# Kernel tuning notes

Hardware: AMD Instinct MI355X
Metric: run time of the kernel (lower is better)

## Reference

```python
import jax, jax.numpy as jnp
import numpy as np

B = 8192
N_COLS = 64
D = 1024
EPS = 1e-5


def _layernorm(x, g, b):
    m = jnp.mean(x, axis=-1, keepdims=True)
    v = jnp.mean(jnp.square(x - m), axis=-1, keepdims=True)
    return (x - m) * jax.lax.rsqrt(v + EPS) * g + b


def setup_inputs() -> dict:
    key = jax.random.key(0)
    ks = jax.random.split(key, 8)
    s = 0.02
    return {
        "x1_enc": jax.random.normal(ks[0], (1, N_COLS, D), jnp.float32),
        "x2_enc": jax.random.normal(ks[1], (B, D), jnp.float32),
        "We": jax.random.normal(ks[2], (4, 2 * D, D), jnp.float32) * s,
        "be": jnp.zeros((4, D), jnp.float32),
        "W1": jax.random.normal(ks[3], (2 * D, 4 * D), jnp.float32) * s,
        "b1": jnp.zeros((4 * D,), jnp.float32),
        "g1": jnp.ones((4 * D,), jnp.float32),
        "bt1": jnp.zeros((4 * D,), jnp.float32),
        "W2": jax.random.normal(ks[4], (4 * D, 2 * D), jnp.float32) * s,
        "b2": jnp.zeros((2 * D,), jnp.float32),
        "g2": jnp.ones((2 * D,), jnp.float32),
        "bt2": jnp.zeros((2 * D,), jnp.float32),
        "W3": jax.random.normal(ks[5], (2 * D, 1), jnp.float32) * s,
        "b3": jnp.zeros((1,), jnp.float32),
        "col_pairs": jax.random.randint(ks[6], (B, 2), 0, N_COLS, jnp.int64),
        "vis_type": jax.random.randint(ks[7], (B,), 0, 4, jnp.int64),
    }


def reference(x1_enc, x2_enc, We, be, W1, b1, g1, bt1, W2, b2, g2, bt2, W3, b3,
              col_pairs, vis_type):
    # x1 repeated B times is identical per row -> gather directly from x1_enc[0]
    x11 = x1_enc[0, col_pairs[:, 0]]          # [B, D]
    x12 = x1_enc[0, col_pairs[:, 1]]          # [B, D]
    x1c = jnp.concatenate([x11, x12], axis=1)  # [B, 2D]

    # 1-of-4 expert routing: compute all experts, select by vis_type
    all_y = jax.nn.relu(jnp.einsum('bd,edk->bek', x1c, We) + be)  # [B, 4, D]
    y1 = jnp.take_along_axis(all_y, vis_type[:, None, None], axis=1)[:, 0]  # [B, D]

    y = jnp.concatenate([y1, x2_enc], axis=1)  # [B, 2D]
    h = _layernorm(jax.nn.relu(y @ W1 + b1), g1, bt1)
    h = _layernorm(jax.nn.relu(h @ W2 + b2), g2, bt2)
    return jax.nn.sigmoid(h @ W3 + b3)  # [B, 1]
```

## Files before the change

### kernel.cpp

```cpp
#include <hip/hip_runtime.h>

typedef unsigned short u16;
typedef __bf16 bf16x8 __attribute__((ext_vector_type(8)));
typedef float f32x4v __attribute__((ext_vector_type(4)));
typedef u16 u16x8 __attribute__((ext_vector_type(8)));

__device__ __forceinline__ u16 f2bf(float f) {
  union { float f; unsigned u; } v; v.f = f;
  unsigned r = v.u + 0x7fffu + ((v.u >> 16) & 1u);
  return (u16)(r >> 16);
}
__device__ __forceinline__ float bf2f(u16 h) {
  union { unsigned u; float f; } v; v.u = ((unsigned)h) << 16;
  return v.f;
}

#define G2L16(g, l)                                                            \
  __builtin_amdgcn_global_load_lds((__attribute__((address_space(1))) void*)(g), \
                                   (__attribute__((address_space(3))) void*)(l), 16, 0, 0)

__global__ __launch_bounds__(256) void k_transpose2(const float* __restrict__ W1,
                                                    u16* __restrict__ W1T,
                                                    const float* __restrict__ W2,
                                                    u16* __restrict__ W2gT,
                                                    const float* __restrict__ g1,
                                                    const float* __restrict__ bt1,
                                                    float* __restrict__ w2ps,
                                                    float* __restrict__ w2pc) {
  __shared__ float tile[64][65];
  int bid = blockIdx.x;
  const float* in;
  u16* out;
  int R, C, bx, by, fold;
  if (bid < 2048) {
    in = W1; out = W1T; R = 2048; C = 4096; fold = 0;
    bx = bid & 63; by = bid >> 6;
  } else {
    bid -= 2048;
    in = W2; out = W2gT; R = 4096; C = 2048; fold = 1;
    bx = bid & 31; by = bid >> 5;
  }
  const int c0 = bx * 64, r0 = by * 64;
  const int t = threadIdx.x;
  const int tc = (t & 15) * 4, tr = t >> 4;
#pragma unroll
  for (int i = 0; i < 4; ++i) {
    int r = tr + i * 16;
    f32x4v v = *(const f32x4v*)(in + (size_t)(r0 + r) * C + c0 + tc);
    tile[r][tc] = v[0]; tile[r][tc + 1] = v[1];
    tile[r][tc + 2] = v[2]; tile[r][tc + 3] = v[3];
  }
  __syncthreads();
  const int oc = t >> 2;
  const int rb = (t & 3) * 16;
  float gv[16];
#pragma unroll
  for (int i = 0; i < 16; ++i) gv[i] = fold ? g1[r0 + rb + i] : 1.f;
  u16x8 o0, o1;
#pragma unroll
  for (int i = 0; i < 8; ++i) o0[i] = f2bf(tile[rb + i][oc] * gv[i]);
#pragma unroll
  for (int i = 0; i < 8; ++i) o1[i] = f2bf(tile[rb + 8 + i][oc] * gv[8 + i]);
  *(u16x8*)(out + (size_t)(c0 + oc) * R + r0 + rb) = o0;
  *(u16x8*)(out + (size_t)(c0 + oc) * R + r0 + rb + 8) = o1;
  if (fold) {
    float ps = 0.f, pc = 0.f;
#pragma unroll
    for (int i = 0; i < 16; ++i) {
      float w = tile[rb + i][oc];
      ps += gv[i] * w;
      pc += bt1[r0 + rb + i] * w;
    }
    ps += __shfl_down(ps, 2, 4); ps += __shfl_down(ps, 1, 4);
    pc += __shfl_down(pc, 2, 4); pc += __shfl_down(pc, 1, 4);
    if ((t & 3) == 0) {
      w2ps[(size_t)by * 2048 + c0 + oc] = ps;
      w2pc[(size_t)by * 2048 + c0 + oc] = pc;
    }
  }
}

__global__ __launch_bounds__(256) void k_pq(const float* __restrict__ x1,
                                            const float* __restrict__ We,
                                            float* __restrict__ pq0,
                                            float* __restrict__ pq1) {
  const int n0 = blockIdx.x * 64;
  const int ep = blockIdx.y;
  const int e = ep >> 1, p = ep & 1;
  const int khalf = blockIdx.z & 1;
  const int chalf = blockIdx.z >> 1;
  const int ks = khalf * 512;
  float* pq = khalf ? pq1 : pq0;
  __shared__ float As[32][33];
  __shared__ float Bs[32][68];
  const int t = threadIdx.x;
  const int tx = t & 15, ty = t >> 4;
  float acc[2][4] = {};
  const float* wbase = We + (size_t)e * 2048 * 1024 + (size_t)p * 1024 * 1024;
  for (int k0 = ks; k0 < ks + 512; k0 += 32) {
#pragma unroll
    for (int i = 0; i < 4; ++i) {
      int ix = t + i * 256;
      As[ix >> 5][ix & 31] =
          x1[(size_t)(chalf * 32 + (ix >> 5)) * 1024 + k0 + (ix & 31)];
    }
#pragma unroll
    for (int i = 0; i < 8; ++i) {
      int ix = t + i * 256;
      Bs[ix >> 6][ix & 63] = wbase[(size_t)(k0 + (ix >> 6)) * 1024 + n0 + (ix & 63)];
    }
    __syncthreads();
#pragma unroll
    for (int kk = 0; kk < 32; ++kk) {
      float av[2];
#pragma unroll
      for (int i = 0; i < 2; ++i) av[i] = As[ty * 2 + i][kk];
      f32x4v bv = *(const f32x4v*)&Bs[kk][tx * 4];
#pragma unroll
      for (int i = 0; i < 2; ++i)
#pragma unroll
        for (int j = 0; j < 4; ++j) acc[i][j] += av[i] * bv[j];
    }
    __syncthreads();
  }
#pragma unroll
  for (int i = 0; i < 2; ++i) {
    float* dst = pq + ((size_t)ep * 64 + chalf * 32 + ty * 2 + i) * 1024 + n0 + tx * 4;
#pragma unroll
    for (int j = 0; j < 4; ++j) dst[j] = acc[i][j];
  }
}

__global__ __launch_bounds__(256) void k_build_y(const float* __restrict__ pq0,
                                                 const float* __restrict__ pq1,
                                                 const float* __restrict__ x2,
                                                 const float* __restrict__ be,
                                                 const int* __restrict__ cp,
                                                 const int* __restrict__ vis,
                                                 u16* __restrict__ Y) {
  const int t = threadIdx.x;
  for (int rr = 0; rr < 8; ++rr) {
    const int b = blockIdx.x * 8 + rr;
    const int e = vis[b];
    u16x8 o;
    if (t < 128) {
      const int c0 = cp[2 * b], c1 = cp[2 * b + 1];
      const size_t po = ((size_t)(e * 2) * 64 + c0) * 1024 + t * 8;
      const size_t qo = ((size_t)(e * 2 + 1) * 64 + c1) * 1024 + t * 8;
      const float* B = be + e * 1024 + t * 8;
#pragma unroll
      for (int i = 0; i < 8; ++i) {
        float v = pq0[po + i] + pq1[po + i] + pq0[qo + i] + pq1[qo + i] + B[i];
        o[i] = f2bf(v > 0.f ? v : 0.f);
      }
      *(u16x8*)(Y + (size_t)b * 2048 + t * 8) = o;
    } else {
      const float* X = x2 + (size_t)b * 1024 + (size_t)(t - 128) * 8;
#pragma unroll
      for (int i = 0; i < 8; ++i) o[i] = f2bf(X[i]);
      *(u16x8*)(Y + (size_t)b * 2048 + 1024 + (size_t)(t - 128) * 8) = o;
    }
  }
}

template <int MODE>
__global__ __launch_bounds__(256, 3) void k_gemm(const u16* __restrict__ A,
                                                 const u16* __restrict__ BT,
                                                 const float* __restrict__ bias,
                                                 const float2* __restrict__ stats,
                                                 const float* __restrict__ s1,
                                                 const float* __restrict__ c1b,
                                                 const float* __restrict__ gw3,
                                                 float2* __restrict__ sp_out,
                                                 float4* __restrict__ part,
                                                 u16* __restrict__ C,
                                                 int M, int N, int K) {
  __shared__ u16 As[128 * 64];
  __shared__ u16 Bs[128 * 64];
  const int tid = threadIdx.x;
  const int lane = tid & 63;
  const int wave = tid >> 6;

  const int nx = gridDim.x, ny = gridDim.y;
  const int bid = blockIdx.y * nx + blockIdx.x;
  const int stripe = ny >> 3;
  const int xcd = bid & 7;
  const int loc = bid >> 3;
  const int panel = loc / (stripe * 4);
  const int rem = loc - panel * (stripe * 4);
  const int by = xcd * stripe + (rem >> 2);
  const int bx = panel * 4 + (rem & 3);
  const int tileN = bx * 128;
  const int tileM = by * 128;
  const int wm = wave & 1;
  const int wn = wave >> 1;

  f32x4v acc[4][4];
#pragma unroll
  for (int i = 0; i < 4; ++i)
#pragma unroll
    for (int j = 0; j < 4; ++j) acc[i][j] = (f32x4v){0.f, 0.f, 0.f, 0.f};

  const int srow = tid >> 3;
  const int lchunk = (tid & 7) ^ (srow & 7);
  const u16* aptr = A + (size_t)(tileM + srow) * K + lchunk * 8;
  const u16* bptr = BT + (size_t)(tileN + srow) * K + lchunk * 8;
  u16* asp = As + tid * 8;
  u16* bsp = Bs + tid * 8;

  const int s = lane & 7;
  const int kp0 = ((lane >> 4) ^ s) * 8;
  const int kp1 = kp0 ^ 32;
  const int am = wm * 64 + (lane & 15);
  const int bn = wn * 64 + (lane & 15);

  for (int k0 = 0; k0 < K; k0 += 64) {
    G2L16(aptr, asp);
    G2L16(aptr + (size_t)32 * K, asp + 2048);
    G2L16(aptr + (size_t)64 * K, asp + 4096);
    G2L16(aptr + (size_t)96 * K, asp + 6144);
    G2L16(bptr, bsp);
    G2L16(bptr + (size_t)32 * K, bsp + 2048);
    G2L16(bptr + (size_t)64 * K, bsp + 4096);
    G2L16(bptr + (size_t)96 * K, bsp + 6144);
    aptr += 64;
    bptr += 64;
    __syncthreads();

    bf16x8 af[4], bfr[4];
#pragma unroll
    for (int mi = 0; mi < 4; ++mi)
      af[mi] = *(const bf16x8*)(As + (am + mi * 16) * 64 + kp0);
#pragma unroll
    for (int ni = 0; ni < 4; ++ni)
      bfr[ni] = *(const bf16x8*)(Bs + (bn + ni * 16) * 64 + kp0);
#pragma unroll
    for (int mi = 0; mi < 4; ++mi)
#pragma unroll
      for (int ni = 0; ni < 4; ++ni)
        acc[mi][ni] = __builtin_amdgcn_mfma_f32_16x16x32_bf16(af[mi], bfr[ni], acc[mi][ni], 0, 0, 0);
#pragma unroll
    for (int mi = 0; mi < 4; ++mi)
      af[mi] = *(const bf16x8*)(As + (am + mi * 16) * 64 + kp1);
#pragma unroll
    for (int ni = 0; ni < 4; ++ni)
      bfr[ni] = *(const bf16x8*)(Bs + (bn + ni * 16) * 64 + kp1);
#pragma unroll
    for (int mi = 0; mi < 4; ++mi)
#pragma unroll
      for (int ni = 0; ni < 4; ++ni)
        acc[mi][ni] = __builtin_amdgcn_mfma_f32_16x16x32_bf16(af[mi], bfr[ni], acc[mi][ni], 0, 0, 0);
    __syncthreads();
  }

  const int crow = tileM + wm * 64 + (lane >> 4) * 4;
  const int ccol = tileN + wn * 64 + (lane & 15);
  float cv0[4], cv1[4], cg[4];
#pragma unroll
  for (int ni = 0; ni < 4; ++ni) {
    const int c = ccol + ni * 16;
    if (MODE == 0) {
      cv0[ni] = bias[c];
    } else {
      cv0[ni] = s1[c];
      cv1[ni] = c1b[c];
      cg[ni] = gw3[c];
    }
  }
  const int cb = bx * 2 + wn;
#pragma unroll
  for (int mi = 0; mi < 4; ++mi) {
#pragma unroll
    for (int r = 0; r < 4; ++r) {
      const int row = crow + mi * 16 + r;
      if (MODE == 0) {
        float s_ = 0.f, ss_ = 0.f;
#pragma unroll
        for (int ni = 0; ni < 4; ++ni) {
          float v = acc[mi][ni][r] + cv0[ni];
          v = v > 0.f ? v : 0.f;
          s_ += v; ss_ += v * v;
          C[(size_t)row * N + ccol + ni * 16] = f2bf(v);
        }
#pragma unroll
        for (int off = 8; off >= 1; off >>= 1) {
          s_ += __shfl_xor(s_, off, 16);
          ss_ += __shfl_xor(ss_, off, 16);
        }
        if ((lane & 15) == 0)
          sp_out[(size_t)row * 64 + cb] = make_float2(s_, ss_);
      } else {
        float2 st = stats[row];
        const float m = st.x, rs = st.y;
        float s_ = 0.f, ss_ = 0.f, d_ = 0.f;
#pragma unroll
        for (int ni = 0; ni < 4; ++ni) {
          float v = rs * acc[mi][ni][r] - rs * m * cv0[ni] + cv1[ni];
          v = v > 0.f ? v : 0.f;
          s_ += v; ss_ += v * v; d_ += v * cg[ni];
        }
#pragma unroll
        for (int off = 8; off >= 1; off >>= 1) {
          s_ += __shfl_xor(s_, off, 16);
          ss_ += __shfl_xor(ss_, off, 16);
          d_ += __shfl_xor(d_, off, 16);
        }
        if ((lane & 15) == 0)
          part[(size_t)row * 32 + cb] = make_float4(s_, ss_, d_, 0.f);
      }
    }
  }
}

__global__ __launch_bounds__(256) void k_reduce(const float2* __restrict__ sp,
                                                float2* __restrict__ stats,
                                                const float* __restrict__ w2ps,
                                                const float* __restrict__ w2pc,
                                                const float* __restrict__ b2,
                                                float* __restrict__ s1,
                                                float* __restrict__ c1b,
                                                const float* __restrict__ g2,
                                                const float* __restrict__ bt2,
                                                const float* __restrict__ W3,
                                                float* __restrict__ gw3,
                                                float* __restrict__ scal) {
  __shared__ float red[8];
  const int bid = blockIdx.x;
  const int t = threadIdx.x;
  if (bid < 32) {
    const int g = t >> 4, l = t & 15;
#pragma unroll 1
    for (int rr = 0; rr < 16; ++rr) {
      const int row = bid * 256 + rr * 16 + g;
      float s = 0.f, ss = 0.f;
#pragma unroll
      for (int i = 0; i < 4; ++i) {
        float2 p = sp[(size_t)row * 64 + l * 4 + i];
        s += p.x; ss += p.y;
      }
#pragma unroll
      for (int off = 8; off >= 1; off >>= 1) {
        s += __shfl_xor(s, off, 16);
        ss += __shfl_xor(ss, off, 16);
      }
      if (l == 0) {
        float m = s * (1.f / 4096.f);
        float var = ss * (1.f / 4096.f) - m * m;
        stats[row] = make_float2(m, rsqrtf(var + 1e-5f));
      }
    }
  } else if (bid < 40) {
    const int nn = (bid - 32) * 256 + t;
    float s = 0.f, c = 0.f;
    for (int kb = 0; kb < 64; ++kb) {
      s += w2ps[(size_t)kb * 2048 + nn];
      c += w2pc[(size_t)kb * 2048 + nn];
    }
    s1[nn] = s;
    c1b[nn] = c + b2[nn];
  } else {
    float sg = 0.f, cb = 0.f;
    for (int i = 0; i < 8; ++i) {
      int c = i * 256 + t;
      float w3 = W3[c];
      float gv = g2[c] * w3;
      gw3[c] = gv;
      sg += gv;
      cb += bt2[c] * w3;
    }
#pragma unroll
    for (int off = 32; off > 0; off >>= 1) {
      sg += __shfl_down(sg, off, 64);
      cb += __shfl_down(cb, off, 64);
    }
    const int lane = t & 63, wv = t >> 6;
    if (lane == 0) { red[wv] = sg; red[4 + wv] = cb; }
    __syncthreads();
    if (t == 0) {
      scal[0] = red[0] + red[1] + red[2] + red[3];
      scal[1] = red[4] + red[5] + red[6] + red[7];
    }
  }
}

__global__ __launch_bounds__(256) void k_final(const float4* __restrict__ part,
                                               const float* __restrict__ scal,
                                               const float* __restrict__ b3,
                                               float* __restrict__ out) {
  const int t = threadIdx.x;
  const int g = t >> 4, l = t & 15;
  const int row = blockIdx.x * 16 + g;
  float4 a = part[(size_t)row * 32 + l * 2];
  float4 b = part[(size_t)row * 32 + l * 2 + 1];
  float S = a.x + b.x, SS = a.y + b.y, D = a.z + b.z;
#pragma unroll
  for (int off = 8; off >= 1; off >>= 1) {
    S += __shfl_xor(S, off, 16);
    SS += __shfl_xor(SS, off, 16);
    D += __shfl_xor(D, off, 16);
  }
  if (l == 0) {
    float m = S * (1.f / 2048.f);
    float rs = rsqrtf(SS * (1.f / 2048.f) - m * m + 1e-5f);
    float logit = rs * D - rs * m * scal[0] + scal[1] + b3[0];
    out[row] = 1.f / (1.f + expf(-logit));
  }
}

extern "C" void kernel_launch(void* const* d_in, const int* in_sizes, int n_in,
                              void* d_out, int out_size, void* d_ws, size_t ws_size,
                              hipStream_t stream) {
  const float* x1 = (const float*)d_in[0];
  const float* x2 = (const float*)d_in[1];
  const float* We = (const float*)d_in[2];
  const float* be = (const float*)d_in[3];
  const float* W1 = (const float*)d_in[4];
  const float* b1 = (const float*)d_in[5];
  const float* g1 = (const float*)d_in[6];
  const float* bt1 = (const float*)d_in[7];
  const float* W2 = (const float*)d_in[8];
  const float* b2 = (const float*)d_in[9];
  const float* g2 = (const float*)d_in[10];
  const float* bt2 = (const float*)d_in[11];
  const float* W3 = (const float*)d_in[12];
  const float* b3 = (const float*)d_in[13];
  const int* cp = (const int*)d_in[14];
  const int* vis = (const int*)d_in[15];
  float* out = (float*)d_out;

  char* ws = (char*)d_ws;
  u16* W1T  = (u16*)(ws);
  u16* W2gT = (u16*)(ws + 16777216);
  u16* Y    = (u16*)(ws + 33554432);
  u16* H1   = (u16*)(ws + 67108864);
  float* PQ0 = (float*)(ws + 134217728);
  float* PQ1 = (float*)(ws + 136314880);
  float2* sp = (float2*)(ws + 134217728);
  float4* part = (float4*)(ws + 134217728);
  float2* stats = (float2*)(ws + 138412032);
  float* s1   = (float*)(ws + 138477568);
  float* c1b  = (float*)(ws + 138485760);
  float* w2ps = (float*)(ws + 138493952);
  float* w2pc = (float*)(ws + 139018240);
  float* gw3  = (float*)(ws + 139542528);
  float* scal = (float*)(ws + 139550720);

  k_transpose2<<<4096, 256, 0, stream>>>(W1, W1T, W2, W2gT, g1, bt1, w2ps, w2pc);
  k_pq<<<dim3(16, 8, 4), 256, 0, stream>>>(x1, We, PQ0, PQ1);
  k_build_y<<<1024, 256, 0, stream>>>(PQ0, PQ1, x2, be, cp, vis, Y);
  k_gemm<0><<<dim3(32, 64), 256, 0, stream>>>(
      Y, W1T, b1, nullptr, nullptr, nullptr, nullptr, sp, nullptr, H1,
      8192, 4096, 2048);
  k_reduce<<<41, 256, 0, stream>>>(sp, stats, w2ps, w2pc, b2, s1, c1b,
                                   g2, bt2, W3, gw3, scal);
  k_gemm<1><<<dim3(16, 64), 256, 0, stream>>>(
      H1, W2gT, nullptr, stats, s1, c1b, gw3, nullptr, part, nullptr,
      8192, 2048, 4096);
  k_final<<<512, 256, 0, stream>>>(part, scal, b3, out);
}
```

Before: 482.9 us.

## Rewrite GEMM as 256x256-tile, 8-wave, double-buffered pipelined kernel

The bf16 MFMA GEMM moves from 128x128 tiles with 4 waves and a single LDS buffer to 256x256 tiles with 8 waves and two LDS buffers. Global-to-LDS loads for the next k-tile are issued while MFMA quadrants run, with explicit vmcnt/lgkmcnt waits, raw barriers and setprio. The aim is to hide load latency and raise operand reuse per block. The cost is 128KB of LDS per block, more registers and fewer blocks in the grid, and the hand-tuned waits could introduce races.

After: 452.7 us. 6.3% less time.

```diff
diff --git a/kernel.cpp b/kernel.cpp
--- a/kernel.cpp
+++ b/kernel.cpp
@@ -163,8 +163,16 @@
   }
 }
 
+#define BARRIER __builtin_amdgcn_s_barrier()
+#define WLG0                                                    \
+  do {                                                          \
+    asm volatile("s_waitcnt lgkmcnt(0)" ::: "memory");          \
+    __builtin_amdgcn_sched_barrier(0);                          \
+  } while (0)
+#define WVM(n) asm volatile("s_waitcnt vmcnt(" #n ")" ::: "memory")
+
 template <int MODE>
-__global__ __launch_bounds__(256, 3) void k_gemm(const u16* __restrict__ A,
+__global__ __launch_bounds__(512, 2) void k_gemm(const u16* __restrict__ A,
                                                  const u16* __restrict__ BT,
                                                  const float* __restrict__ bias,
                                                  const float2* __restrict__ stats,
@@ -175,85 +183,119 @@
                                                  float4* __restrict__ part,
                                                  u16* __restrict__ C,
                                                  int M, int N, int K) {
-  __shared__ u16 As[128 * 64];
-  __shared__ u16 Bs[128 * 64];
+  __shared__ u16 smem[65536];
   const int tid = threadIdx.x;
   const int lane = tid & 63;
   const int wave = tid >> 6;
+  const int wm = wave >> 2;
+  const int wn = wave & 3;
 
   const int nx = gridDim.x, ny = gridDim.y;
   const int bid = blockIdx.y * nx + blockIdx.x;
   const int stripe = ny >> 3;
   const int xcd = bid & 7;
   const int loc = bid >> 3;
-  const int panel = loc / (stripe * 4);
-  const int rem = loc - panel * (stripe * 4);
-  const int by = xcd * stripe + (rem >> 2);
-  const int bx = panel * 4 + (rem & 3);
-  const int tileN = bx * 128;
-  const int tileM = by * 128;
-  const int wm = wave & 1;
-  const int wn = wave >> 1;
-
-  f32x4v acc[4][4];
-#pragma unroll
-  for (int i = 0; i < 4; ++i)
+  const int by = xcd * stripe + (loc % stripe);
+  const int bx = loc / stripe;
+  const int tileM = by * 256;
+  const int tileN = bx * 256;
+
+  f32x4v acc[8][4];
+#pragma unroll
+  for (int i = 0; i < 8; ++i)
 #pragma unroll
     for (int j = 0; j < 4; ++j) acc[i][j] = (f32x4v){0.f, 0.f, 0.f, 0.f};
 
   const int srow = tid >> 3;
-  const int lchunk = (tid & 7) ^ (srow & 7);
-  const u16* aptr = A + (size_t)(tileM + srow) * K + lchunk * 8;
-  const u16* bptr = BT + (size_t)(tileN + srow) * K + lchunk * 8;
-  u16* asp = As + tid * 8;
-  u16* bsp = Bs + tid * 8;
-
-  const int s = lane & 7;
-  const int kp0 = ((lane >> 4) ^ s) * 8;
+  const int slc = ((tid & 7) ^ (srow & 7)) * 8;
+  const u16* aG = A + (size_t)(tileM + srow) * K + slc;
+  const u16* bG = BT + (size_t)(tileN + srow) * K + slc;
+
+#define STAGE(ab, h, buf, kt)                                                  \
+  do {                                                                         \
+    u16* dst_ = smem + (buf) * 32768 + (ab) * 16384 + (h) * 8192 + tid * 8;    \
+    const u16* g_ = ((ab) ? bG : aG) + (size_t)(h) * 128 * K + (size_t)(kt) * 64; \
+    G2L16(g_, dst_);                                                           \
+    G2L16(g_ + (size_t)64 * K, dst_ + 4096);                                   \
+  } while (0)
+
+  const int kp0 = (((lane >> 4) ^ (lane & 7)) * 8);
   const int kp1 = kp0 ^ 32;
-  const int am = wm * 64 + (lane & 15);
-  const int bn = wn * 64 + (lane & 15);
-
-  for (int k0 = 0; k0 < K; k0 += 64) {
-    G2L16(aptr, asp);
-    G2L16(aptr + (size_t)32 * K, asp + 2048);
-    G2L16(aptr + (size_t)64 * K, asp + 4096);
-    G2L16(aptr + (size_t)96 * K, asp + 6144);
-    G2L16(bptr, bsp);
-    G2L16(bptr + (size_t)32 * K, bsp + 2048);
-    G2L16(bptr + (size_t)64 * K, bsp + 4096);
-    G2L16(bptr + (size_t)96 * K, bsp + 6144);
-    aptr += 64;
-    bptr += 64;
-    __syncthreads();
-
-    bf16x8 af[4], bfr[4];
-#pragma unroll
-    for (int mi = 0; mi < 4; ++mi)
-      af[mi] = *(const bf16x8*)(As + (am + mi * 16) * 64 + kp0);
-#pragma unroll
-    for (int ni = 0; ni < 4; ++ni)
-      bfr[ni] = *(const bf16x8*)(Bs + (bn + ni * 16) * 64 + kp0);
-#pragma unroll
-    for (int mi = 0; mi < 4; ++mi)
-#pragma unroll
-      for (int ni = 0; ni < 4; ++ni)
-        acc[mi][ni] = __builtin_amdgcn_mfma_f32_16x16x32_bf16(af[mi], bfr[ni], acc[mi][ni], 0, 0, 0);
-#pragma unroll
-    for (int mi = 0; mi < 4; ++mi)
-      af[mi] = *(const bf16x8*)(As + (am + mi * 16) * 64 + kp1);
-#pragma unroll
-    for (int ni = 0; ni < 4; ++ni)
-      bfr[ni] = *(const bf16x8*)(Bs + (bn + ni * 16) * 64 + kp1);
-#pragma unroll
-    for (int mi = 0; mi < 4; ++mi)
-#pragma unroll
-      for (int ni = 0; ni < 4; ++ni)
-        acc[mi][ni] = __builtin_amdgcn_mfma_f32_16x16x32_bf16(af[mi], bfr[ni], acc[mi][ni], 0, 0, 0);
-    __syncthreads();
-  }
-
-  const int crow = tileM + wm * 64 + (lane >> 4) * 4;
+  const int awoff = wm * 8192 + (lane & 15) * 64;
+  const int bwoff = (wn >> 1) * 8192 + ((wn & 1) * 64 + (lane & 15)) * 64;
+
+  bf16x8 af[2][4], bf[2][4];
+
+#define RD_A(buf, mh)                                                          \
+  do {                                                                         \
+    const u16* ap_ = smem + (buf) * 32768 + awoff;                             \
+    _Pragma("unroll") for (int q = 0; q < 4; ++q) {                            \
+      af[0][q] = *(const bf16x8*)(ap_ + ((mh) * 4 + q) * 1024 + kp0);          \
+      af[1][q] = *(const bf16x8*)(ap_ + ((mh) * 4 + q) * 1024 + kp1);          \
+    }                                                                          \
+  } while (0)
+
+#define RD_B(buf, nh)                                                          \
+  do {                                                                         \
+    const u16* bp_ = smem + (buf) * 32768 + 16384 + bwoff;                     \
+    _Pragma("unroll") for (int q = 0; q < 2; ++q) {                            \
+      bf[0][(nh) * 2 + q] = *(const bf16x8*)(bp_ + ((nh) * 2 + q) * 1024 + kp0); \
+      bf[1][(nh) * 2 + q] = *(const bf16x8*)(bp_ + ((nh) * 2 + q) * 1024 + kp1); \
+    }                                                                          \
+  } while (0)
+
+#define QUAD(mh, nh)                                                           \
+  do {                                                                         \
+    __builtin_amdgcn_s_setprio(1);                                             \
+    _Pragma("unroll") for (int kh = 0; kh < 2; ++kh)                           \
+    _Pragma("unroll") for (int q = 0; q < 4; ++q)                              \
+    _Pragma("unroll") for (int p = 0; p < 2; ++p)                              \
+      acc[(mh) * 4 + q][(nh) * 2 + p] = __builtin_amdgcn_mfma_f32_16x16x32_bf16( \
+          af[kh][q], bf[kh][(nh) * 2 + p], acc[(mh) * 4 + q][(nh) * 2 + p], 0, 0, 0); \
+    __builtin_amdgcn_s_setprio(0);                                             \
+  } while (0)
+
+  const int nkt = K >> 6;
+  const int niter = nkt >> 1;
+
+  STAGE(1, 0, 0, 0);
+  STAGE(1, 1, 0, 0);
+  STAGE(0, 0, 0, 0);
+  STAGE(0, 1, 0, 0);
+  STAGE(1, 0, 1, 1);
+  STAGE(1, 1, 1, 1);
+  WVM(4);
+  BARRIER;
+
+  for (int it = 0; it < niter; ++it) {
+    const int t1 = 2 * it + 1;
+    int t2 = 2 * it + 2; if (t2 >= nkt) t2 = nkt - 1;
+    int t3 = 2 * it + 3; if (t3 >= nkt) t3 = nkt - 1;
+    RD_A(0, 0); RD_B(0, 0);
+    STAGE(0, 0, 1, t1);
+    BARRIER; WLG0; QUAD(0, 0); BARRIER;
+    RD_B(0, 1);
+    STAGE(0, 1, 1, t1);
+    BARRIER; WLG0; QUAD(0, 1); BARRIER;
+    RD_A(0, 1);
+    STAGE(1, 0, 0, t2);
+    BARRIER; WLG0; QUAD(1, 0); BARRIER;
+    STAGE(1, 1, 0, t2);
+    BARRIER; QUAD(1, 1); WVM(4); BARRIER;
+    RD_A(1, 0); RD_B(1, 0);
+    STAGE(0, 0, 0, t2);
+    BARRIER; WLG0; QUAD(0, 0); BARRIER;
+    RD_B(1, 1);
+    STAGE(0, 1, 0, t2);
+    BARRIER; WLG0; QUAD(0, 1); BARRIER;
+    RD_A(1, 1);
+    STAGE(1, 0, 1, t3);
+    BARRIER; WLG0; QUAD(1, 0); BARRIER;
+    STAGE(1, 1, 1, t3);
+    BARRIER; QUAD(1, 1); WVM(4); BARRIER;
+  }
+
+  const int crow = tileM + wm * 128 + (lane >> 4) * 4;
   const int ccol = tileN + wn * 64 + (lane & 15);
   float cv0[4], cv1[4], cg[4];
 #pragma unroll
@@ -267,9 +309,9 @@
       cg[ni] = gw3[c];
     }
   }
-  const int cb = bx * 2 + wn;
-#pragma unroll
-  for (int mi = 0; mi < 4; ++mi) {
+  const int cb = bx * 4 + wn;
+#pragma unroll
+  for (int mi = 0; mi < 8; ++mi) {
 #pragma unroll
     for (int r = 0; r < 4; ++r) {
       const int row = crow + mi * 16 + r;
@@ -448,12 +490,12 @@
   k_transpose2<<<4096, 256, 0, stream>>>(W1, W1T, W2, W2gT, g1, bt1, w2ps, w2pc);
   k_pq<<<dim3(16, 8, 4), 256, 0, stream>>>(x1, We, PQ0, PQ1);
   k_build_y<<<1024, 256, 0, stream>>>(PQ0, PQ1, x2, be, cp, vis, Y);
-  k_gemm<0><<<dim3(32, 64), 256, 0, stream>>>(
+  k_gemm<0><<<dim3(16, 32), 512, 0, stream>>>(
       Y, W1T, b1, nullptr, nullptr, nullptr, nullptr, sp, nullptr, H1,
       8192, 4096, 2048);
   k_reduce<<<41, 256, 0, stream>>>(sp, stats, w2ps, w2pc, b2, s1, c1b,
                                    g2, bt2, W3, gw3, scal);
-  k_gemm<1><<<dim3(16, 64), 256, 0, stream>>>(
+  k_gemm<1><<<dim3(8, 32), 512, 0, stream>>>(
       H1, W2gT, nullptr, stats, s1, c1b, gw3, nullptr, part, nullptr,
       8192, 2048, 4096);
   k_final<<<512, 256, 0, stream>>>(part, scal, b3, out);
```
